# Performance work log

Measured on AMD Instinct MI355X. Metric: run time of the kernel, lower is better.

Reference implementation:

```python
import jax, jax.numpy as jnp
import numpy as np

INPUT_DIM = 128
HIDDEN_DIM = 128
WINDOW_SIZE = 256
BLOCK_SIZE = 256
BATCH = 8
SEQ = 8192


def setup_inputs() -> dict:
    key = jax.random.key(0)
    ks = jax.random.split(key, 7)
    s = 1.0 / np.sqrt(INPUT_DIM)
    return {
        "x": jax.random.normal(ks[0], (BATCH, SEQ, INPUT_DIM), dtype=jnp.float32),
        "Wq": jax.random.normal(ks[1], (HIDDEN_DIM, INPUT_DIM), dtype=jnp.float32) * s,
        "bq": jax.random.normal(ks[2], (HIDDEN_DIM,), dtype=jnp.float32) * s,
        "Wk": jax.random.normal(ks[3], (HIDDEN_DIM, INPUT_DIM), dtype=jnp.float32) * s,
        "bk": jax.random.normal(ks[4], (HIDDEN_DIM,), dtype=jnp.float32) * s,
        "Wv": jax.random.normal(ks[5], (HIDDEN_DIM, INPUT_DIM), dtype=jnp.float32) * s,
        "bv": jax.random.normal(ks[6], (HIDDEN_DIM,), dtype=jnp.float32) * s,
    }


def reference(x, Wq, bq, Wk, bk, Wv, bv):
    B, S, D = x.shape
    bs, w = BLOCK_SIZE, WINDOW_SIZE
    nb = S // bs
    halo = w - 1
    W = bs + 2 * halo  # per-block K/V window width

    q = x @ Wq.T + bq  # [B,S,H]
    k = x @ Wk.T + bk
    v = x @ Wv.T + bv

    # Zero-pad K/V by halo on both sides. Since there is NO softmax, padded
    # zero keys give zero scores and padded zero values contribute zero —
    # this exactly reproduces the torch code's clamped window slicing.
    k_pad = jnp.pad(k, ((0, 0), (halo, halo), (0, 0)))
    v_pad = jnp.pad(v, ((0, 0), (halo, halo), (0, 0)))

    # Gather overlapping windows: [B, nb, W, H]
    starts = jnp.arange(nb) * bs  # window start in padded coords
    idx = starts[:, None] + jnp.arange(W)[None, :]  # [nb, W]
    k_win = k_pad[:, idx, :]
    v_win = v_pad[:, idx, :]

    q_blk = q.reshape(B, nb, bs, -1)  # [B, nb, bs, H]

    scale = 1.0 / jnp.sqrt(jnp.float32(D))
    attn = jnp.einsum('bnqh,bnkh->bnqk', q_blk, k_win) * scale  # no softmax
    out = jnp.einsum('bnqk,bnkh->bnqh', attn, v_win)
    return out.reshape(B, S, -1)
```

## Files before the change

### kernel.cpp

```cpp
#include <hip/hip_runtime.h>
#include <stdint.h>


#define B_ 8
#define S_ 8192
#define LDW 136
#define LDT 264

using bf16x8 = __attribute__((ext_vector_type(8))) short;
using s16x4  = __attribute__((ext_vector_type(4))) short;
using f32x16 = __attribute__((ext_vector_type(16))) float;

__device__ __forceinline__ short f2bf(float f) {
  union { float f; uint32_t u; } v; v.f = f;
  uint32_t r = v.u + 0x7fffu + ((v.u >> 16) & 1u);
  return (short)(r >> 16);
}
__device__ __forceinline__ float bf2f(short s) {
  union { uint32_t u; float f; } v; v.u = ((uint32_t)(uint16_t)s) << 16;
  return v.f;
}

__global__ __launch_bounds__(512) void kv_kernel(
    const float* __restrict__ x,
    const float* __restrict__ Wq, const float* __restrict__ bq,
    const float* __restrict__ Wk, const float* __restrict__ bk,
    const float* __restrict__ Wv, const float* __restrict__ bv,
    short* __restrict__ qb, float* __restrict__ Cpart,
    short* __restrict__ kedge, short* __restrict__ vedge)
{
  __shared__ __align__(16) char smem[137216];
  short* rgA = (short*)smem;
  short* rgB = (short*)(smem + 69632);

  const int tid  = threadIdx.x;
  const int lane = tid & 63;
  const int wv   = tid >> 6;
  const int c    = lane & 31;
  const int hl   = lane >> 5;
  const int r0   = blockIdx.x * 256;
  const int b    = r0 >> 13;
  const int n    = (r0 & (S_ - 1)) >> 8;

  bf16x8 afrag[8];
  {
    const float* xrow = x + (size_t)(r0 + wv * 32 + c) * 128 + hl * 8;
    #pragma unroll
    for (int kst = 0; kst < 8; ++kst) {
      const float4* p = (const float4*)(xrow + kst * 16);
      float4 f0 = p[0], f1 = p[1];
      bf16x8 a;
      a[0] = f2bf(f0.x); a[1] = f2bf(f0.y); a[2] = f2bf(f0.z); a[3] = f2bf(f0.w);
      a[4] = f2bf(f1.x); a[5] = f2bf(f1.y); a[6] = f2bf(f1.z); a[7] = f2bf(f1.w);
      afrag[kst] = a;
    }
  }

  auto stageW = [&](const float* W, short* wl) {
    #pragma unroll
    for (int it = 0; it < 8; ++it) {
      int l  = it * 512 + tid;
      int nn = l >> 5;
      int k4 = (l & 31) << 2;
      const float4 f = *(const float4*)(W + nn * 128 + k4);
      s16x4 o;
      o[0] = f2bf(f.x); o[1] = f2bf(f.y); o[2] = f2bf(f.z); o[3] = f2bf(f.w);
      *(s16x4*)(wl + nn * LDW + k4) = o;
    }
  };

  auto gemm = [&](const float* bias, f32x16* acc, const short* wl) {
    #pragma unroll
    for (int nt = 0; nt < 4; ++nt) {
      float bvv = bias[nt * 32 + c];
      #pragma unroll
      for (int i = 0; i < 16; ++i) acc[nt][i] = bvv;
    }
    #pragma unroll
    for (int kst = 0; kst < 8; ++kst) {
      #pragma unroll
      for (int nt = 0; nt < 4; ++nt) {
        bf16x8 bb = *(const bf16x8*)(wl + (nt * 32 + c) * LDW + kst * 16 + hl * 8);
        acc[nt] = __builtin_amdgcn_mfma_f32_32x32x16_bf16(afrag[kst], bb, acc[nt], 0, 0, 0);
      }
    }
  };

  auto writeTransposedLDS = [&](f32x16* acc, short* wl) {
    #pragma unroll
    for (int nt = 0; nt < 4; ++nt) {
      int d = nt * 32 + c;
      #pragma unroll
      for (int g = 0; g < 4; ++g) {
        #pragma unroll
        for (int p = 0; p < 2; ++p) {
          int reg = g * 4 + p * 2;
          int sl  = wv * 32 + g * 8 + hl * 4 + p * 2;
          uint32_t pk = (uint32_t)(uint16_t)f2bf(acc[nt][reg]) |
                        ((uint32_t)(uint16_t)f2bf(acc[nt][reg + 1]) << 16);
          *(uint32_t*)(wl + d * LDT + sl) = pk;
        }
      }
    }
  };

  stageW(Wq, rgA);
  __syncthreads();
  f32x16 qacc[4];
  gemm(bq, qacc, rgA);
  __syncthreads();

  #pragma unroll
  for (int nt = 0; nt < 4; ++nt) {
    #pragma unroll
    for (int reg = 0; reg < 16; ++reg) {
      int row = (reg & 3) + 8 * (reg >> 2) + 4 * hl;
      rgA[(wv * 32 + row) * LDW + nt * 32 + c] = f2bf(qacc[nt][reg]);
    }
  }
  stageW(Wk, rgB);
  __syncthreads();

  #pragma unroll
  for (int it = 0; it < 8; ++it) {
    int l  = it * 512 + tid;
    int s  = l >> 4;
    int d8 = (l & 15) << 3;
    bf16x8 vvv = *(const bf16x8*)(rgA + s * LDW + d8);
    *(bf16x8*)(qb + (size_t)(r0 + s) * 128 + d8) = vvv;
  }
  f32x16 kacc[4];
  gemm(bk, kacc, rgB);
  __syncthreads();

  writeTransposedLDS(kacc, rgA);
  stageW(Wv, rgB);
  __syncthreads();

  f32x16 vacc[4];
  gemm(bv, vacc, rgB);
  __syncthreads();

  writeTransposedLDS(vacc, rgB);
  __syncthreads();

  {
    const int ht = wv >> 1;
    const int dh = wv & 1;
    f32x16 cacc[2];
    #pragma unroll
    for (int t = 0; t < 2; ++t)
      #pragma unroll
      for (int i = 0; i < 16; ++i) cacc[t][i] = 0.f;

    #pragma unroll
    for (int kst = 0; kst < 16; ++kst) {
      bf16x8 a  = *(const bf16x8*)(rgB + (ht * 32 + c) * LDT + kst * 16 + hl * 8);
      bf16x8 b0 = *(const bf16x8*)(rgA + (dh * 64 + c) * LDT + kst * 16 + hl * 8);
      bf16x8 b1 = *(const bf16x8*)(rgA + (dh * 64 + 32 + c) * LDT + kst * 16 + hl * 8);
      cacc[0] = __builtin_amdgcn_mfma_f32_32x32x16_bf16(a, b0, cacc[0], 0, 0, 0);
      cacc[1] = __builtin_amdgcn_mfma_f32_32x32x16_bf16(a, b1, cacc[1], 0, 0, 0);
    }

    {
      size_t eo = ((size_t)(b * 32 + n)) * 256;
      if (tid < 128)      kedge[eo + tid]               = rgA[tid * LDT + 0];
      else if (tid < 256) kedge[eo + 128 + (tid - 128)] = rgA[(tid - 128) * LDT + 255];
      else if (tid < 384) vedge[eo + (tid - 256)]       = rgB[(tid - 256) * LDT + 0];
      else                vedge[eo + 128 + (tid - 384)] = rgB[(tid - 384) * LDT + 255];
    }

    float* Cp = Cpart + ((size_t)(b * 32 + n)) * 16384;
    #pragma unroll
    for (int t = 0; t < 2; ++t) {
      #pragma unroll
      for (int reg = 0; reg < 16; ++reg) {
        int row = (reg & 3) + 8 * (reg >> 2) + 4 * hl;
        Cp[(ht * 32 + row) * 128 + dh * 64 + t * 32 + c] = cacc[t][reg];
      }
    }
  }
}

__global__ __launch_bounds__(512) void attn_kernel(
    const short* __restrict__ qb, const float* __restrict__ Cpart,
    const short* __restrict__ kedge, const short* __restrict__ vedge,
    float* __restrict__ out)
{
  __shared__ __align__(16) short m_l[128 * LDW];
  __shared__ __align__(16) float opat[8 * 32 * 36];

  const int tid  = threadIdx.x;
  const int lane = tid & 63;
  const int wv   = tid >> 6;
  const int c    = lane & 31;
  const int hl   = lane >> 5;
  const int r0   = blockIdx.x * 256;
  const int b    = r0 >> 13;
  const int n    = (r0 & (S_ - 1)) >> 8;

  float m[32];
  #pragma unroll
  for (int i = 0; i < 32; ++i) m[i] = 0.f;

  const float* Cb0 = Cpart + (size_t)b * 32 * 16384;
  #pragma unroll
  for (int e = 0; e < 3; ++e) {
    int nn = n - 1 + e;
    if (nn < 0 || nn > 31) continue;
    const float4* Cp = (const float4*)(Cb0 + (size_t)nn * 16384);
    #pragma unroll
    for (int i4 = 0; i4 < 8; ++i4) {
      float4 f = Cp[i4 * 512 + tid];
      m[i4 * 4 + 0] += f.x; m[i4 * 4 + 1] += f.y;
      m[i4 * 4 + 2] += f.z; m[i4 * 4 + 3] += f.w;
    }
  }

  const int d0 = (tid & 31) << 2;
  if (n > 0) {
    const short* ke = kedge + ((size_t)(b * 32 + n - 1)) * 256;
    const short* ve = vedge + ((size_t)(b * 32 + n - 1)) * 256;
    float k0 = bf2f(ke[d0]),     k1 = bf2f(ke[d0 + 1]);
    float k2 = bf2f(ke[d0 + 2]), k3 = bf2f(ke[d0 + 3]);
    #pragma unroll
    for (int i4 = 0; i4 < 8; ++i4) {
      float vs = bf2f(ve[i4 * 16 + (tid >> 5)]);
      m[i4 * 4 + 0] -= vs * k0; m[i4 * 4 + 1] -= vs * k1;
      m[i4 * 4 + 2] -= vs * k2; m[i4 * 4 + 3] -= vs * k3;
    }
  }
  if (n < 31) {
    const short* ke = kedge + ((size_t)(b * 32 + n + 1)) * 256 + 128;
    const short* ve = vedge + ((size_t)(b * 32 + n + 1)) * 256 + 128;
    float k0 = bf2f(ke[d0]),     k1 = bf2f(ke[d0 + 1]);
    float k2 = bf2f(ke[d0 + 2]), k3 = bf2f(ke[d0 + 3]);
    #pragma unroll
    for (int i4 = 0; i4 < 8; ++i4) {
      float vs = bf2f(ve[i4 * 16 + (tid >> 5)]);
      m[i4 * 4 + 0] -= vs * k0; m[i4 * 4 + 1] -= vs * k1;
      m[i4 * 4 + 2] -= vs * k2; m[i4 * 4 + 3] -= vs * k3;
    }
  }

  const float scale = 0.08838834764831845f;
  #pragma unroll
  for (int i4 = 0; i4 < 8; ++i4) {
    int h = i4 * 16 + (tid >> 5);
    s16x4 o;
    o[0] = f2bf(m[i4 * 4 + 0] * scale); o[1] = f2bf(m[i4 * 4 + 1] * scale);
    o[2] = f2bf(m[i4 * 4 + 2] * scale); o[3] = f2bf(m[i4 * 4 + 3] * scale);
    *(s16x4*)(m_l + h * LDW + d0) = o;
  }

  bf16x8 qf[8];
  {
    const short* q0p = qb + (size_t)(r0 + wv * 32 + c) * 128 + hl * 8;
    #pragma unroll
    for (int kst = 0; kst < 8; ++kst) qf[kst] = *(const bf16x8*)(q0p + kst * 16);
  }
  __syncthreads();

  f32x16 oacc[4];
  #pragma unroll
  for (int nt = 0; nt < 4; ++nt)
    #pragma unroll
    for (int i = 0; i < 16; ++i) oacc[nt][i] = 0.f;

  #pragma unroll
  for (int kst = 0; kst < 8; ++kst) {
    #pragma unroll
    for (int nt = 0; nt < 4; ++nt) {
      bf16x8 bb = *(const bf16x8*)(m_l + (nt * 32 + c) * LDW + kst * 16 + hl * 8);
      oacc[nt] = __builtin_amdgcn_mfma_f32_32x32x16_bf16(qf[kst], bb, oacc[nt], 0, 0, 0);
    }
  }

  float* patch = opat + wv * (32 * 36);
  float* outb  = out + ((size_t)b * S_ + n * 256 + wv * 32) * 128;
  #pragma unroll
  for (int nt = 0; nt < 4; ++nt) {
    #pragma unroll
    for (int reg = 0; reg < 16; ++reg) {
      int row = (reg & 3) + 8 * (reg >> 2) + 4 * hl;
      patch[row * 36 + c] = oacc[nt][reg];
    }
    #pragma unroll
    for (int p = 0; p < 4; ++p) {
      int row = p * 8 + (lane >> 3);
      float4 vv = *(const float4*)(patch + row * 36 + (lane & 7) * 4);
      *(float4*)(outb + (size_t)row * 128 + nt * 32 + (lane & 7) * 4) = vv;
    }
  }
}

extern "C" void kernel_launch(void* const* d_in, const int* in_sizes, int n_in,
                              void* d_out, int out_size, void* d_ws, size_t ws_size,
                              hipStream_t stream) {
  const float* x  = (const float*)d_in[0];
  const float* Wq = (const float*)d_in[1];
  const float* bq = (const float*)d_in[2];
  const float* Wk = (const float*)d_in[3];
  const float* bk = (const float*)d_in[4];
  const float* Wv = (const float*)d_in[5];
  const float* bv = (const float*)d_in[6];
  float* out = (float*)d_out;

  float* Cpart = (float*)d_ws;
  short* kedge = (short*)(Cpart + (size_t)8 * 32 * 16384);
  short* vedge = kedge + (size_t)8 * 32 * 256;
  short* qb    = vedge + (size_t)8 * 32 * 256;

  kv_kernel<<<256, 512, 0, stream>>>(x, Wq, bq, Wk, bk, Wv, bv,
                                     qb, Cpart, kedge, vedge);
  attn_kernel<<<256, 512, 0, stream>>>(qb, Cpart, kedge, vedge, out);
}
```

Before: 118.5 us.

## Fuse KV and attention kernels, recomputing neighbor-block K/V projections per workgroup

Merges the two kernels into one. Each workgroup now recomputes the K and V projections for its whole window (up to three blocks, in 128-row chunks) and accumulates V^T K directly, instead of writing per-block partial products, edge rows and Q to global memory and reading them back in a second launch. Block indices are also remapped across the batch. This removes the global intermediate traffic and one launch, at the cost of roughly three times the K/V projection work per workgroup and extra barriers inside the loop.

```diff
diff --git a/kernel.cpp b/kernel.cpp
--- a/kernel.cpp
+++ b/kernel.cpp
@@ -5,7 +5,7 @@
 #define B_ 8
 #define S_ 8192
 #define LDW 136
-#define LDT 264
+#define LDH 136
 
 using bf16x8 = __attribute__((ext_vector_type(8))) short;
 using s16x4  = __attribute__((ext_vector_type(4))) short;
@@ -16,45 +16,47 @@
   uint32_t r = v.u + 0x7fffu + ((v.u >> 16) & 1u);
   return (short)(r >> 16);
 }
-__device__ __forceinline__ float bf2f(short s) {
-  union { uint32_t u; float f; } v; v.u = ((uint32_t)(uint16_t)s) << 16;
-  return v.f;
-}
-
-__global__ __launch_bounds__(512) void kv_kernel(
+
+__global__ __launch_bounds__(512) void fused_kernel(
     const float* __restrict__ x,
     const float* __restrict__ Wq, const float* __restrict__ bq,
     const float* __restrict__ Wk, const float* __restrict__ bk,
     const float* __restrict__ Wv, const float* __restrict__ bv,
-    short* __restrict__ qb, float* __restrict__ Cpart,
-    short* __restrict__ kedge, short* __restrict__ vedge)
+    float* __restrict__ out)
 {
-  __shared__ __align__(16) char smem[137216];
-  short* rgA = (short*)smem;
-  short* rgB = (short*)(smem + 69632);
+  __shared__ __align__(16) char smem[139264];
+  short* area1 = (short*)smem;
+  short* area2 = (short*)(smem + 34816);
+  short* ktile = (short*)(smem + 69632);
+  short* vtile = (short*)(smem + 104448);
+  short* q_l   = (short*)(smem + 69632);
+  short* m_l   = (short*)(smem + 34816);
+  float* opat  = (float*)(smem + 69632);
 
   const int tid  = threadIdx.x;
   const int lane = tid & 63;
   const int wv   = tid >> 6;
   const int c    = lane & 31;
   const int hl   = lane >> 5;
-  const int r0   = blockIdx.x * 256;
+  const int wg   = ((int)blockIdx.x & 7) * 32 + ((int)blockIdx.x >> 3);
+  const int r0   = wg * 256;
   const int b    = r0 >> 13;
   const int n    = (r0 & (S_ - 1)) >> 8;
-
-  bf16x8 afrag[8];
-  {
-    const float* xrow = x + (size_t)(r0 + wv * 32 + c) * 128 + hl * 8;
-    #pragma unroll
-    for (int kst = 0; kst < 8; ++kst) {
-      const float4* p = (const float4*)(xrow + kst * 16);
+  const int rg   = wv >> 1;
+  const int dh   = wv & 1;
+
+  auto loadA = [&](bf16x8* af, int row0) {
+    const float* xr = x + ((size_t)row0 + c) * 128 + hl * 8;
+    #pragma unroll
+    for (int kst = 0; kst < 8; ++kst) {
+      const float4* p = (const float4*)(xr + kst * 16);
       float4 f0 = p[0], f1 = p[1];
       bf16x8 a;
       a[0] = f2bf(f0.x); a[1] = f2bf(f0.y); a[2] = f2bf(f0.z); a[3] = f2bf(f0.w);
       a[4] = f2bf(f1.x); a[5] = f2bf(f1.y); a[6] = f2bf(f1.z); a[7] = f2bf(f1.w);
-      afrag[kst] = a;
-    }
-  }
+      af[kst] = a;
+    }
+  };
 
   auto stageW = [&](const float* W, short* wl) {
     #pragma unroll
@@ -69,45 +71,80 @@
     }
   };
 
-  auto gemm = [&](const float* bias, f32x16* acc, const short* wl) {
-    #pragma unroll
-    for (int nt = 0; nt < 4; ++nt) {
-      float bvv = bias[nt * 32 + c];
-      #pragma unroll
-      for (int i = 0; i < 16; ++i) acc[nt][i] = bvv;
-    }
-    #pragma unroll
-    for (int kst = 0; kst < 8; ++kst) {
-      #pragma unroll
-      for (int nt = 0; nt < 4; ++nt) {
-        bf16x8 bb = *(const bf16x8*)(wl + (nt * 32 + c) * LDW + kst * 16 + hl * 8);
-        acc[nt] = __builtin_amdgcn_mfma_f32_32x32x16_bf16(afrag[kst], bb, acc[nt], 0, 0, 0);
-      }
-    }
-  };
-
-  auto writeTransposedLDS = [&](f32x16* acc, short* wl) {
-    #pragma unroll
-    for (int nt = 0; nt < 4; ++nt) {
-      int d = nt * 32 + c;
+  auto projHalf = [&](const float* bias, f32x16* acc, const short* wl,
+                      const bf16x8* af) {
+    #pragma unroll
+    for (int t = 0; t < 2; ++t) {
+      float bvv = bias[(2 * dh + t) * 32 + c];
+      #pragma unroll
+      for (int i = 0; i < 16; ++i) acc[t][i] = bvv;
+    }
+    #pragma unroll
+    for (int kst = 0; kst < 8; ++kst) {
+      #pragma unroll
+      for (int t = 0; t < 2; ++t) {
+        bf16x8 bb = *(const bf16x8*)(wl + ((2 * dh + t) * 32 + c) * LDW +
+                                     kst * 16 + hl * 8);
+        acc[t] = __builtin_amdgcn_mfma_f32_32x32x16_bf16(af[kst], bb, acc[t], 0, 0, 0);
+      }
+    }
+  };
+
+  auto transpHalf = [&](f32x16* acc, short* tile, bool eL, bool eR) {
+    #pragma unroll
+    for (int t = 0; t < 2; ++t) {
+      int d = (2 * dh + t) * 32 + c;
       #pragma unroll
       for (int g = 0; g < 4; ++g) {
         #pragma unroll
         for (int p = 0; p < 2; ++p) {
           int reg = g * 4 + p * 2;
-          int sl  = wv * 32 + g * 8 + hl * 4 + p * 2;
-          uint32_t pk = (uint32_t)(uint16_t)f2bf(acc[nt][reg]) |
-                        ((uint32_t)(uint16_t)f2bf(acc[nt][reg + 1]) << 16);
-          *(uint32_t*)(wl + d * LDT + sl) = pk;
+          int sl  = rg * 32 + g * 8 + hl * 4 + p * 2;
+          uint32_t pk = (uint32_t)(uint16_t)f2bf(acc[t][reg]) |
+                        ((uint32_t)(uint16_t)f2bf(acc[t][reg + 1]) << 16);
+          if (eL && sl == 0)   pk &= 0xFFFF0000u;
+          if (eR && sl == 126) pk &= 0x0000FFFFu;
+          *(uint32_t*)(tile + d * LDH + sl) = pk;
         }
       }
     }
   };
 
-  stageW(Wq, rgA);
-  __syncthreads();
+  auto cgemm = [&](f32x16* mc) {
+    #pragma unroll
+    for (int kst = 0; kst < 8; ++kst) {
+      bf16x8 a = *(const bf16x8*)(vtile + (rg * 32 + c) * LDH + kst * 16 + hl * 8);
+      #pragma unroll
+      for (int t = 0; t < 2; ++t) {
+        bf16x8 bb = *(const bf16x8*)(ktile + (dh * 64 + t * 32 + c) * LDH +
+                                     kst * 16 + hl * 8);
+        mc[t] = __builtin_amdgcn_mfma_f32_32x32x16_bf16(a, bb, mc[t], 0, 0, 0);
+      }
+    }
+  };
+
+  bf16x8 afA[8];
+  loadA(afA, r0 + wv * 32);
+  stageW(Wq, area1);
+  __syncthreads();
+
   f32x16 qacc[4];
-  gemm(bq, qacc, rgA);
+  {
+    #pragma unroll
+    for (int nt = 0; nt < 4; ++nt) {
+      float bvv = bq[nt * 32 + c];
+      #pragma unroll
+      for (int i = 0; i < 16; ++i) qacc[nt][i] = bvv;
+    }
+    #pragma unroll
+    for (int kst = 0; kst < 8; ++kst) {
+      #pragma unroll
+      for (int nt = 0; nt < 4; ++nt) {
+        bf16x8 bb = *(const bf16x8*)(area1 + (nt * 32 + c) * LDW + kst * 16 + hl * 8);
+        qacc[nt] = __builtin_amdgcn_mfma_f32_32x32x16_bf16(afA[kst], bb, qacc[nt], 0, 0, 0);
+      }
+    }
+  }
   __syncthreads();
 
   #pragma unroll
@@ -115,149 +152,68 @@
     #pragma unroll
     for (int reg = 0; reg < 16; ++reg) {
       int row = (reg & 3) + 8 * (reg >> 2) + 4 * hl;
-      rgA[(wv * 32 + row) * LDW + nt * 32 + c] = f2bf(qacc[nt][reg]);
-    }
-  }
-  stageW(Wk, rgB);
-  __syncthreads();
-
-  #pragma unroll
-  for (int it = 0; it < 8; ++it) {
-    int l  = it * 512 + tid;
-    int s  = l >> 4;
-    int d8 = (l & 15) << 3;
-    bf16x8 vvv = *(const bf16x8*)(rgA + s * LDW + d8);
-    *(bf16x8*)(qb + (size_t)(r0 + s) * 128 + d8) = vvv;
-  }
-  f32x16 kacc[4];
-  gemm(bk, kacc, rgB);
-  __syncthreads();
-
-  writeTransposedLDS(kacc, rgA);
-  stageW(Wv, rgB);
-  __syncthreads();
-
-  f32x16 vacc[4];
-  gemm(bv, vacc, rgB);
-  __syncthreads();
-
-  writeTransposedLDS(vacc, rgB);
-  __syncthreads();
-
-  {
-    const int ht = wv >> 1;
-    const int dh = wv & 1;
-    f32x16 cacc[2];
-    #pragma unroll
-    for (int t = 0; t < 2; ++t)
-      #pragma unroll
-      for (int i = 0; i < 16; ++i) cacc[t][i] = 0.f;
-
-    #pragma unroll
-    for (int kst = 0; kst < 16; ++kst) {
-      bf16x8 a  = *(const bf16x8*)(rgB + (ht * 32 + c) * LDT + kst * 16 + hl * 8);
-      bf16x8 b0 = *(const bf16x8*)(rgA + (dh * 64 + c) * LDT + kst * 16 + hl * 8);
-      bf16x8 b1 = *(const bf16x8*)(rgA + (dh * 64 + 32 + c) * LDT + kst * 16 + hl * 8);
-      cacc[0] = __builtin_amdgcn_mfma_f32_32x32x16_bf16(a, b0, cacc[0], 0, 0, 0);
-      cacc[1] = __builtin_amdgcn_mfma_f32_32x32x16_bf16(a, b1, cacc[1], 0, 0, 0);
-    }
-
-    {
-      size_t eo = ((size_t)(b * 32 + n)) * 256;
-      if (tid < 128)      kedge[eo + tid]               = rgA[tid * LDT + 0];
-      else if (tid < 256) kedge[eo + 128 + (tid - 128)] = rgA[(tid - 128) * LDT + 255];
-      else if (tid < 384) vedge[eo + (tid - 256)]       = rgB[(tid - 256) * LDT + 0];
-      else                vedge[eo + 128 + (tid - 384)] = rgB[(tid - 384) * LDT + 255];
-    }
-
-    float* Cp = Cpart + ((size_t)(b * 32 + n)) * 16384;
-    #pragma unroll
-    for (int t = 0; t < 2; ++t) {
-      #pragma unroll
-      for (int reg = 0; reg < 16; ++reg) {
-        int row = (reg & 3) + 8 * (reg >> 2) + 4 * hl;
-        Cp[(ht * 32 + row) * 128 + dh * 64 + t * 32 + c] = cacc[t][reg];
-      }
-    }
-  }
-}
-
-__global__ __launch_bounds__(512) void attn_kernel(
-    const short* __restrict__ qb, const float* __restrict__ Cpart,
-    const short* __restrict__ kedge, const short* __restrict__ vedge,
-    float* __restrict__ out)
-{
-  __shared__ __align__(16) short m_l[128 * LDW];
-  __shared__ __align__(16) float opat[8 * 32 * 36];
-
-  const int tid  = threadIdx.x;
-  const int lane = tid & 63;
-  const int wv   = tid >> 6;
-  const int c    = lane & 31;
-  const int hl   = lane >> 5;
-  const int r0   = blockIdx.x * 256;
-  const int b    = r0 >> 13;
-  const int n    = (r0 & (S_ - 1)) >> 8;
-
-  float m[32];
-  #pragma unroll
-  for (int i = 0; i < 32; ++i) m[i] = 0.f;
-
-  const float* Cb0 = Cpart + (size_t)b * 32 * 16384;
-  #pragma unroll
-  for (int e = 0; e < 3; ++e) {
-    int nn = n - 1 + e;
-    if (nn < 0 || nn > 31) continue;
-    const float4* Cp = (const float4*)(Cb0 + (size_t)nn * 16384);
-    #pragma unroll
-    for (int i4 = 0; i4 < 8; ++i4) {
-      float4 f = Cp[i4 * 512 + tid];
-      m[i4 * 4 + 0] += f.x; m[i4 * 4 + 1] += f.y;
-      m[i4 * 4 + 2] += f.z; m[i4 * 4 + 3] += f.w;
-    }
-  }
-
-  const int d0 = (tid & 31) << 2;
-  if (n > 0) {
-    const short* ke = kedge + ((size_t)(b * 32 + n - 1)) * 256;
-    const short* ve = vedge + ((size_t)(b * 32 + n - 1)) * 256;
-    float k0 = bf2f(ke[d0]),     k1 = bf2f(ke[d0 + 1]);
-    float k2 = bf2f(ke[d0 + 2]), k3 = bf2f(ke[d0 + 3]);
-    #pragma unroll
-    for (int i4 = 0; i4 < 8; ++i4) {
-      float vs = bf2f(ve[i4 * 16 + (tid >> 5)]);
-      m[i4 * 4 + 0] -= vs * k0; m[i4 * 4 + 1] -= vs * k1;
-      m[i4 * 4 + 2] -= vs * k2; m[i4 * 4 + 3] -= vs * k3;
-    }
-  }
-  if (n < 31) {
-    const short* ke = kedge + ((size_t)(b * 32 + n + 1)) * 256 + 128;
-    const short* ve = vedge + ((size_t)(b * 32 + n + 1)) * 256 + 128;
-    float k0 = bf2f(ke[d0]),     k1 = bf2f(ke[d0 + 1]);
-    float k2 = bf2f(ke[d0 + 2]), k3 = bf2f(ke[d0 + 3]);
-    #pragma unroll
-    for (int i4 = 0; i4 < 8; ++i4) {
-      float vs = bf2f(ve[i4 * 16 + (tid >> 5)]);
-      m[i4 * 4 + 0] -= vs * k0; m[i4 * 4 + 1] -= vs * k1;
-      m[i4 * 4 + 2] -= vs * k2; m[i4 * 4 + 3] -= vs * k3;
-    }
-  }
+      q_l[(wv * 32 + row) * LDW + nt * 32 + c] = f2bf(qacc[nt][reg]);
+    }
+  }
+  stageW(Wk, area1);
+  stageW(Wv, area2);
+  const int jlo = (n == 0) ? 0 : 2 * n - 2;
+  const int jhi = (n == 31) ? 64 : 2 * n + 4;
+  loadA(afA, b * S_ + jlo * 128 + rg * 32);
+  __syncthreads();
+
+  bf16x8 qf[8];
+  #pragma unroll
+  for (int kst = 0; kst < 8; ++kst)
+    qf[kst] = *(const bf16x8*)(q_l + (wv * 32 + c) * LDW + kst * 16 + hl * 8);
+
+  f32x16 macc[2];
+  #pragma unroll
+  for (int t = 0; t < 2; ++t)
+    #pragma unroll
+    for (int i = 0; i < 16; ++i) macc[t][i] = 0.f;
+
+  for (int jj = jlo; jj < jhi; jj += 2) {
+    bf16x8 afB[8];
+    loadA(afB, b * S_ + (jj + 1) * 128 + rg * 32);
+    {
+      f32x16 ka[2];
+      projHalf(bk, ka, area1, afA);
+      __syncthreads();
+      transpHalf(ka, ktile, jj == 2 * n - 2, false);
+    }
+    {
+      f32x16 va[2];
+      projHalf(bv, va, area2, afA);
+      transpHalf(va, vtile, false, false);
+    }
+    __syncthreads();
+    cgemm(macc);
+    if (jj + 2 < jhi) loadA(afA, b * S_ + (jj + 2) * 128 + rg * 32);
+    {
+      f32x16 kb[2];
+      projHalf(bk, kb, area1, afB);
+      __syncthreads();
+      transpHalf(kb, ktile, false, jj + 1 == 2 * n + 3);
+    }
+    {
+      f32x16 vb[2];
+      projHalf(bv, vb, area2, afB);
+      transpHalf(vb, vtile, false, false);
+    }
+    __syncthreads();
+    cgemm(macc);
+  }
+  __syncthreads();
 
   const float scale = 0.08838834764831845f;
   #pragma unroll
-  for (int i4 = 0; i4 < 8; ++i4) {
-    int h = i4 * 16 + (tid >> 5);
-    s16x4 o;
-    o[0] = f2bf(m[i4 * 4 + 0] * scale); o[1] = f2bf(m[i4 * 4 + 1] * scale);
-    o[2] = f2bf(m[i4 * 4 + 2] * scale); o[3] = f2bf(m[i4 * 4 + 3] * scale);
-    *(s16x4*)(m_l + h * LDW + d0) = o;
-  }
-
-  bf16x8 qf[8];
-  {
-    const short* q0p = qb + (size_t)(r0 + wv * 32 + c) * 128 + hl * 8;
-    #pragma unroll
-    for (int kst = 0; kst < 8; ++kst) qf[kst] = *(const bf16x8*)(q0p + kst * 16);
+  for (int t = 0; t < 2; ++t) {
+    #pragma unroll
+    for (int reg = 0; reg < 16; ++reg) {
+      int row = (reg & 3) + 8 * (reg >> 2) + 4 * hl;
+      m_l[(rg * 32 + row) * LDW + dh * 64 + t * 32 + c] = f2bf(macc[t][reg] * scale);
+    }
   }
   __syncthreads();
 
@@ -277,7 +233,7 @@
   }
 
   float* patch = opat + wv * (32 * 36);
-  float* outb  = out + ((size_t)b * S_ + n * 256 + wv * 32) * 128;
+  float* outb  = out + ((size_t)r0 + wv * 32) * 128;
   #pragma unroll
   for (int nt = 0; nt < 4; ++nt) {
     #pragma unroll
@@ -306,12 +262,5 @@
   const float* bv = (const float*)d_in[6];
   float* out = (float*)d_out;
 
-  float* Cpart = (float*)d_ws;
-  short* kedge = (short*)(Cpart + (size_t)8 * 32 * 16384);
-  short* vedge = kedge + (size_t)8 * 32 * 256;
-  short* qb    = vedge + (size_t)8 * 32 * 256;
-
-  kv_kernel<<<256, 512, 0, stream>>>(x, Wq, bq, Wk, bk, Wv, bv,
-                                     qb, Cpart, kedge, vedge);
-  attn_kernel<<<256, 512, 0, stream>>>(qb, Cpart, kedge, vedge, out);
+  fused_kernel<<<256, 512, 0, stream>>>(x, Wq, bq, Wk, bk, Wv, bv, out);
 }
```

After: 136.9 us. +15.5%, slower.

## Split KV projection into 128-row half-blocks and swizzle attention block order

Applied to the files above, without the earlier changes.

The KV/projection kernel now processes 128-row chunks with 256 threads over 512 workgroups instead of 256-row chunks with 512 threads. This cuts shared memory per block, so more blocks can be resident and the grid covers more of the GPU. Each half-block writes its own partial K^T V matrix, so the attention kernel now sums six partials instead of three, which doubles Cpart traffic. The attention kernel also remaps block indices so consecutive blocks fall in different batches, which may change cache locality.

```diff
diff --git a/kernel.cpp b/kernel.cpp
--- a/kernel.cpp
+++ b/kernel.cpp
@@ -5,7 +5,6 @@
 #define B_ 8
 #define S_ 8192
 #define LDW 136
-#define LDT 264
 
 using bf16x8 = __attribute__((ext_vector_type(8))) short;
 using s16x4  = __attribute__((ext_vector_type(4))) short;
@@ -21,7 +20,7 @@
   return v.f;
 }
 
-__global__ __launch_bounds__(512) void kv_kernel(
+__global__ __launch_bounds__(256) void kv_kernel(
     const float* __restrict__ x,
     const float* __restrict__ Wq, const float* __restrict__ bq,
     const float* __restrict__ Wk, const float* __restrict__ bk,
@@ -29,18 +28,17 @@
     short* __restrict__ qb, float* __restrict__ Cpart,
     short* __restrict__ kedge, short* __restrict__ vedge)
 {
-  __shared__ __align__(16) char smem[137216];
-  short* rgA = (short*)smem;
-  short* rgB = (short*)(smem + 69632);
+  __shared__ __align__(16) short areaA[128 * LDW];
+  __shared__ __align__(16) short areaB[128 * LDW];
 
   const int tid  = threadIdx.x;
   const int lane = tid & 63;
   const int wv   = tid >> 6;
   const int c    = lane & 31;
   const int hl   = lane >> 5;
-  const int r0   = blockIdx.x * 256;
+  const int r0   = blockIdx.x * 128;
   const int b    = r0 >> 13;
-  const int n    = (r0 & (S_ - 1)) >> 8;
+  const int j    = (r0 & (S_ - 1)) >> 7;
 
   bf16x8 afrag[8];
   {
@@ -58,8 +56,8 @@
 
   auto stageW = [&](const float* W, short* wl) {
     #pragma unroll
-    for (int it = 0; it < 8; ++it) {
-      int l  = it * 512 + tid;
+    for (int it = 0; it < 16; ++it) {
+      int l  = it * 256 + tid;
       int nn = l >> 5;
       int k4 = (l & 31) << 2;
       const float4 f = *(const float4*)(W + nn * 128 + k4);
@@ -98,16 +96,17 @@
           int sl  = wv * 32 + g * 8 + hl * 4 + p * 2;
           uint32_t pk = (uint32_t)(uint16_t)f2bf(acc[nt][reg]) |
                         ((uint32_t)(uint16_t)f2bf(acc[nt][reg + 1]) << 16);
-          *(uint32_t*)(wl + d * LDT + sl) = pk;
+          *(uint32_t*)(wl + d * LDW + sl) = pk;
         }
       }
     }
   };
 
-  stageW(Wq, rgA);
-  __syncthreads();
+  stageW(Wq, areaA);
+  __syncthreads();
+
   f32x16 qacc[4];
-  gemm(bq, qacc, rgA);
+  gemm(bq, qacc, areaA);
   __syncthreads();
 
   #pragma unroll
@@ -115,68 +114,67 @@
     #pragma unroll
     for (int reg = 0; reg < 16; ++reg) {
       int row = (reg & 3) + 8 * (reg >> 2) + 4 * hl;
-      rgA[(wv * 32 + row) * LDW + nt * 32 + c] = f2bf(qacc[nt][reg]);
-    }
-  }
-  stageW(Wk, rgB);
+      areaB[(wv * 32 + row) * LDW + nt * 32 + c] = f2bf(qacc[nt][reg]);
+    }
+  }
+  stageW(Wk, areaA);
   __syncthreads();
 
   #pragma unroll
   for (int it = 0; it < 8; ++it) {
-    int l  = it * 512 + tid;
+    int l  = it * 256 + tid;
     int s  = l >> 4;
     int d8 = (l & 15) << 3;
-    bf16x8 vvv = *(const bf16x8*)(rgA + s * LDW + d8);
+    bf16x8 vvv = *(const bf16x8*)(areaB + s * LDW + d8);
     *(bf16x8*)(qb + (size_t)(r0 + s) * 128 + d8) = vvv;
   }
   f32x16 kacc[4];
-  gemm(bk, kacc, rgB);
-  __syncthreads();
-
-  writeTransposedLDS(kacc, rgA);
-  stageW(Wv, rgB);
+  gemm(bk, kacc, areaA);
+  __syncthreads();
+
+  writeTransposedLDS(kacc, areaB);
+  stageW(Wv, areaA);
   __syncthreads();
 
   f32x16 vacc[4];
-  gemm(bv, vacc, rgB);
-  __syncthreads();
-
-  writeTransposedLDS(vacc, rgB);
+  gemm(bv, vacc, areaA);
+  __syncthreads();
+
+  writeTransposedLDS(vacc, areaA);
   __syncthreads();
 
   {
-    const int ht = wv >> 1;
-    const int dh = wv & 1;
-    f32x16 cacc[2];
-    #pragma unroll
-    for (int t = 0; t < 2; ++t)
-      #pragma unroll
-      for (int i = 0; i < 16; ++i) cacc[t][i] = 0.f;
-
-    #pragma unroll
-    for (int kst = 0; kst < 16; ++kst) {
-      bf16x8 a  = *(const bf16x8*)(rgB + (ht * 32 + c) * LDT + kst * 16 + hl * 8);
-      bf16x8 b0 = *(const bf16x8*)(rgA + (dh * 64 + c) * LDT + kst * 16 + hl * 8);
-      bf16x8 b1 = *(const bf16x8*)(rgA + (dh * 64 + 32 + c) * LDT + kst * 16 + hl * 8);
-      cacc[0] = __builtin_amdgcn_mfma_f32_32x32x16_bf16(a, b0, cacc[0], 0, 0, 0);
-      cacc[1] = __builtin_amdgcn_mfma_f32_32x32x16_bf16(a, b1, cacc[1], 0, 0, 0);
+    f32x16 cacc[4];
+    #pragma unroll
+    for (int nt = 0; nt < 4; ++nt)
+      #pragma unroll
+      for (int i = 0; i < 16; ++i) cacc[nt][i] = 0.f;
+
+    #pragma unroll
+    for (int kst = 0; kst < 8; ++kst) {
+      bf16x8 a = *(const bf16x8*)(areaA + (wv * 32 + c) * LDW + kst * 16 + hl * 8);
+      #pragma unroll
+      for (int nt = 0; nt < 4; ++nt) {
+        bf16x8 bb = *(const bf16x8*)(areaB + (nt * 32 + c) * LDW + kst * 16 + hl * 8);
+        cacc[nt] = __builtin_amdgcn_mfma_f32_32x32x16_bf16(a, bb, cacc[nt], 0, 0, 0);
+      }
     }
 
     {
-      size_t eo = ((size_t)(b * 32 + n)) * 256;
-      if (tid < 128)      kedge[eo + tid]               = rgA[tid * LDT + 0];
-      else if (tid < 256) kedge[eo + 128 + (tid - 128)] = rgA[(tid - 128) * LDT + 255];
-      else if (tid < 384) vedge[eo + (tid - 256)]       = rgB[(tid - 256) * LDT + 0];
-      else                vedge[eo + 128 + (tid - 384)] = rgB[(tid - 384) * LDT + 255];
-    }
-
-    float* Cp = Cpart + ((size_t)(b * 32 + n)) * 16384;
-    #pragma unroll
-    for (int t = 0; t < 2; ++t) {
+      const int slot = j & 1;
+      const int col  = slot ? 127 : 0;
+      size_t eo = ((size_t)(b * 32 + (j >> 1))) * 256 + slot * 128;
+      if (tid < 128)      kedge[eo + tid]         = areaB[tid * LDW + col];
+      else                vedge[eo + (tid - 128)] = areaA[(tid - 128) * LDW + col];
+    }
+
+    float* Cp = Cpart + ((size_t)(b * 64 + j)) * 16384;
+    #pragma unroll
+    for (int nt = 0; nt < 4; ++nt) {
       #pragma unroll
       for (int reg = 0; reg < 16; ++reg) {
         int row = (reg & 3) + 8 * (reg >> 2) + 4 * hl;
-        Cp[(ht * 32 + row) * 128 + dh * 64 + t * 32 + c] = cacc[t][reg];
+        Cp[(wv * 32 + row) * 128 + nt * 32 + c] = cacc[nt][reg];
       }
     }
   }
@@ -195,7 +193,8 @@
   const int wv   = tid >> 6;
   const int c    = lane & 31;
   const int hl   = lane >> 5;
-  const int r0   = blockIdx.x * 256;
+  const int wg   = ((int)blockIdx.x & 7) * 32 + ((int)blockIdx.x >> 3);
+  const int r0   = wg * 256;
   const int b    = r0 >> 13;
   const int n    = (r0 & (S_ - 1)) >> 8;
 
@@ -203,12 +202,12 @@
   #pragma unroll
   for (int i = 0; i < 32; ++i) m[i] = 0.f;
 
-  const float* Cb0 = Cpart + (size_t)b * 32 * 16384;
-  #pragma unroll
-  for (int e = 0; e < 3; ++e) {
-    int nn = n - 1 + e;
-    if (nn < 0 || nn > 31) continue;
-    const float4* Cp = (const float4*)(Cb0 + (size_t)nn * 16384);
+  const float* Cb0 = Cpart + (size_t)b * 64 * 16384;
+  #pragma unroll
+  for (int e = 0; e < 6; ++e) {
+    int hj = 2 * n - 2 + e;
+    if (hj < 0 || hj >= 64) continue;
+    const float4* Cp = (const float4*)(Cb0 + (size_t)hj * 16384);
     #pragma unroll
     for (int i4 = 0; i4 < 8; ++i4) {
       float4 f = Cp[i4 * 512 + tid];
@@ -277,7 +276,7 @@
   }
 
   float* patch = opat + wv * (32 * 36);
-  float* outb  = out + ((size_t)b * S_ + n * 256 + wv * 32) * 128;
+  float* outb  = out + ((size_t)r0 + wv * 32) * 128;
   #pragma unroll
   for (int nt = 0; nt < 4; ++nt) {
     #pragma unroll
@@ -307,11 +306,11 @@
   float* out = (float*)d_out;
 
   float* Cpart = (float*)d_ws;
-  short* kedge = (short*)(Cpart + (size_t)8 * 32 * 16384);
+  short* kedge = (short*)(Cpart + (size_t)8 * 64 * 16384);
   short* vedge = kedge + (size_t)8 * 32 * 256;
   short* qb    = vedge + (size_t)8 * 32 * 256;
 
-  kv_kernel<<<256, 512, 0, stream>>>(x, Wq, bq, Wk, bk, Wv, bv,
+  kv_kernel<<<512, 256, 0, stream>>>(x, Wq, bq, Wk, bk, Wv, bv,
                                      qb, Cpart, kedge, vedge);
   attn_kernel<<<256, 512, 0, stream>>>(qb, Cpart, kedge, vedge, out);
 }
```

Result: no change. 119.2 us (+0.5%).
